# Optimization experiments

Measured on AMD Instinct MI355X. Metric: run time of the kernel, lower is better.

The kernel has to match this reference:

```python
import jax, jax.numpy as jnp
import numpy as np

B, C, H, E, K, QT = 256, 1024, 64, 64, 2, 20000

def _mlp(x, W1, b1, W2, b2):
    # GKT MLP (eval mode: dropout off; batch-norm omitted, see notes)
    return jax.nn.relu(jax.nn.relu(x @ W1 + b1) @ W2 + b2)

def setup_inputs() -> dict:
    key = jax.random.key(0)
    ks = jax.random.split(key, 30)
    s = 0.05  # weight scale to keep pre-clamp activations in a sane range
    xt = jax.random.uniform(ks[0], (B,), dtype=jnp.float32)
    qt = jax.random.randint(ks[1], (B,), 0, QT)
    ht = jax.random.normal(ks[2], (B, C, H), dtype=jnp.float32)
    # binary question->concept incidence, ~4 KCs per question, col 0 forced on
    oh = (jax.random.uniform(ks[3], (QT, C)) < 4.0 / C).astype(jnp.float32)
    oh = oh.at[:, 0].set(1.0)
    qt_kc_one_hot = jnp.concatenate([oh, jnp.zeros((1, C), jnp.float32)], axis=0)  # zero padding row
    kc_embeddings = jax.random.normal(ks[4], (C, E), dtype=jnp.float32) * 0.1
    graphs = jax.random.uniform(ks[5], (K, C, C), dtype=jnp.float32)  # graph_model output
    neigh_weight = jnp.float32(0.8)
    MI = H + E
    Ws1 = jax.random.normal(ks[6], (MI, H), jnp.float32) * s; bs1 = jnp.zeros((H,), jnp.float32)
    Ws2 = jax.random.normal(ks[7], (H, H), jnp.float32) * s;  bs2 = jnp.zeros((H,), jnp.float32)
    Wn1 = jax.random.normal(ks[8], (K, 2 * MI, H), jnp.float32) * s; bn1 = jnp.zeros((K, H), jnp.float32)
    Wn2 = jax.random.normal(ks[9], (K, H, H), jnp.float32) * s;      bn2 = jnp.zeros((K, H), jnp.float32)
    ea_w = jax.random.uniform(ks[10], (C,), dtype=jnp.float32)
    We = jax.random.normal(ks[11], (H, H), jnp.float32) * s; be = jnp.zeros((H,), jnp.float32)
    Wa = jax.random.normal(ks[12], (H, H), jnp.float32) * s; ba = jnp.zeros((H,), jnp.float32)
    W_ih = jax.random.normal(ks[13], (H, 3 * H), jnp.float32) * s; b_ih = jnp.zeros((3 * H,), jnp.float32)
    W_hh = jax.random.normal(ks[14], (H, 3 * H), jnp.float32) * s; b_hh = jnp.zeros((3 * H,), jnp.float32)
    Wp = jax.random.normal(ks[15], (H, 1), jnp.float32) * s; bp = jnp.zeros((1,), jnp.float32)
    return dict(xt=xt, qt=qt, ht=ht, qt_kc_one_hot=qt_kc_one_hot, kc_embeddings=kc_embeddings,
                graphs=graphs, neigh_weight=neigh_weight, Ws1=Ws1, bs1=bs1, Ws2=Ws2, bs2=bs2,
                Wn1=Wn1, bn1=bn1, Wn2=Wn2, bn2=bn2, ea_w=ea_w, We=We, be=be, Wa=Wa, ba=ba,
                W_ih=W_ih, b_ih=b_ih, W_hh=W_hh, b_hh=b_hh, Wp=Wp, bp=bp)

def reference(xt, qt, ht, qt_kc_one_hot, kc_embeddings, graphs, neigh_weight,
              Ws1, bs1, Ws2, bs2, Wn1, bn1, Wn2, bn2, ea_w, We, be, Wa, ba,
              W_ih, b_ih, W_hh, b_hh, Wp, bp):
    # ---- _aggregate: the fusion loops never write back, so tmp_ht = cat(ht, kc_emb)
    mask = qt_kc_one_hot[qt]                                   # [B, C] gather of binary incidence
    kc = jnp.broadcast_to(kc_embeddings[None], (mask.shape[0], C, E))
    tmp_ht = jnp.concatenate([ht, kc], axis=-1)                # [B, C, H+E]
    # ---- _agg_neighbors
    self_ht = tmp_ht * mask[..., None]
    self_feat = jnp.clip(_mlp(self_ht, Ws1, bs1, Ws2, bs2), -10.0, 10.0)
    neigh_ht = jnp.clip(jnp.concatenate([self_ht, tmp_ht], axis=-1), -5.0, 5.0)  # [B,C,2(H+E)]
    # bug-faithful adj: mean of graphs[k] rows over sample 0's active concepts
    a0 = mask[0]                                               # [C]
    denom = jnp.maximum(a0.sum(), 1.0)
    adj = jnp.clip(jnp.einsum('c,kcd->kd', a0, graphs) / denom, -5.0, 5.0)       # [K, C]
    nb = jax.vmap(lambda W1, b1, W2, b2: _mlp(neigh_ht, W1, b1, W2, b2))(Wn1, bn1, Wn2, bn2)
    nb = jnp.clip(nb, -5.0, 5.0)                               # [K, B, C, H]
    w = jnp.clip(neigh_weight, 0.1, 0.9)
    nf = jnp.clip(adj[0][None, :, None] * nb[0], -5.0, 5.0)
    for k in range(1, K):
        nf = jnp.clip(w * nf + (1.0 - w) * adj[k][None, :, None] * nb[k], -5.0, 5.0)
    m_next = jnp.clip(jnp.where(mask[..., None] > 0.5, self_feat, nf), -50.0, 50.0)
    # ---- erase-add gate
    g = ea_w[None, :, None]
    res = m_next - g * jax.nn.sigmoid(m_next @ We + be) * m_next + g * jnp.tanh(m_next @ Wa + ba)
    # ---- GRUCell over flattened (B*C) rows
    gi = res @ W_ih + b_ih
    gh = ht @ W_hh + b_hh
    ir, iz, in_ = jnp.split(gi, 3, axis=-1)
    hr, hz, hn = jnp.split(gh, 3, axis=-1)
    r = jax.nn.sigmoid(ir + hr)
    z = jax.nn.sigmoid(iz + hz)
    n = jnp.tanh(in_ + r * hn)
    h_next = (1.0 - z) * n + z * ht                            # [B, C, H]
    y = jax.nn.sigmoid(h_next @ Wp + bp)[..., 0]               # [B, C]
    return y
```

## Files before the change

kernel.cpp:

```cpp
#include <hip/hip_runtime.h>

#define DEVINL __device__ __forceinline__

typedef __bf16 bf16x8 __attribute__((ext_vector_type(8)));
typedef float  f32x4  __attribute__((ext_vector_type(4)));

static constexpr size_t kAdjOff  = 0;
static constexpr size_t kBiasOff = 8192;
static constexpr size_t kFragOff = 8192 + 786432;

static constexpr int FB_Wn1h0 = 0,  FB_Wn1h1 = 8,  FB_Wn2_0 = 16, FB_Wn2_1 = 24;
static constexpr int FB_Ws1h  = 32, FB_Ws2   = 40, FB_We    = 48, FB_Wa    = 56;
static constexpr int FB_Wih   = 64, FB_Whh   = 88;

DEVINL unsigned short bf16r(float f) {
  unsigned u = __builtin_bit_cast(unsigned, f);
  unsigned r = ((u >> 16) & 1u) + 0x7FFFu;
  return (unsigned short)((u + r) >> 16);
}
DEVINL float sigmoidf_(float x) { return __builtin_amdgcn_rcpf(1.f + __expf(-x)); }
DEVINL float tanhf_(float x)    { return 1.f - 2.f * __builtin_amdgcn_rcpf(1.f + __expf(2.f * x)); }

DEVINL void lds_fence() {
  __builtin_amdgcn_sched_barrier(0x7F);
  __builtin_amdgcn_s_waitcnt(0xC07F);
  __builtin_amdgcn_sched_barrier(0x7F);
}

DEVINL f32x4 mfma16(bf16x8 a, bf16x8 b, f32x4 c) {
  return __builtin_amdgcn_mfma_f32_16x16x32_bf16(a, b, c, 0, 0, 0);
}

DEVINL unsigned clip2_(unsigned x) {
  float lo = __builtin_bit_cast(float, x << 16);
  float hi = __builtin_bit_cast(float, x & 0xFFFF0000u);
  lo = fminf(fmaxf(lo, -5.f), 5.f);
  hi = fminf(fmaxf(hi, -5.f), 5.f);
  return (__builtin_bit_cast(unsigned, lo) >> 16) | (__builtin_bit_cast(unsigned, hi) & 0xFFFF0000u);
}
DEVINL bf16x8 clip5(bf16x8 a) {
  uint4 u = __builtin_bit_cast(uint4, a);
  u.x = clip2_(u.x); u.y = clip2_(u.y); u.z = clip2_(u.z); u.w = clip2_(u.w);
  return __builtin_bit_cast(bf16x8, u);
}

__global__ void prep_adj_kernel(const int* __restrict__ qt, const float* __restrict__ onehot,
                                const float* __restrict__ graphs, float* __restrict__ adjw) {
  __shared__ float a0v[1024];
  __shared__ int   aidx[1024];
  __shared__ int   s_nnz;
  __shared__ float s_den;
  const int tid = threadIdx.x;
  const int k = blockIdx.x >> 2, chunk = blockIdx.x & 3;
  if (tid == 0) { s_nnz = 0; s_den = 0.f; }
  __syncthreads();
  const int q0 = qt[0];
  float lsum = 0.f;
#pragma unroll
  for (int i = 0; i < 4; i++) {
    int c = tid * 4 + i;
    float v = onehot[(size_t)q0 * 1024 + c];
    lsum += v;
    if (v != 0.f) { int p = atomicAdd(&s_nnz, 1); aidx[p] = c; a0v[p] = v; }
  }
#pragma unroll
  for (int off = 32; off >= 1; off >>= 1) lsum += __shfl_xor(lsum, off, 64);
  if ((tid & 63) == 0) atomicAdd(&s_den, lsum);
  __syncthreads();
  const float denom = fmaxf(s_den, 1.f);
  const int nnz = s_nnz;
  const int d = chunk * 256 + tid;
  const float* G = graphs + (size_t)k * 1048576 + d;
  float sum = 0.f;
  for (int j = 0; j < nnz; j++) sum += a0v[j] * G[(size_t)aidx[j] * 1024];
  adjw[k * 1024 + d] = fminf(fmaxf(sum / denom, -5.f), 5.f);
}

__global__ void prep_bias_kernel(const float* __restrict__ kc, const float* __restrict__ Wn1,
                                 const float* __restrict__ bn1, const float* __restrict__ Ws1,
                                 const float* __restrict__ bs1, float* __restrict__ biasTab) {
  int gid = blockIdx.x * 256 + threadIdx.x;
  int j = gid & 63;
  int c = (gid >> 6) & 1023;
  int tab = gid >> 16;
  const float* kcr = kc + (size_t)c * 64;
  float s;
  if (tab < 2) {
    s = bn1[tab * 64 + j];
    const float* W = Wn1 + ((size_t)tab * 256 + 192) * 64 + j;
#pragma unroll 4
    for (int e = 0; e < 64; e++) s += fminf(fmaxf(kcr[e], -5.f), 5.f) * W[(size_t)e * 64];
  } else {
    s = bs1[j];
    const float* W = Ws1 + (size_t)64 * 64 + j;
#pragma unroll 4
    for (int e = 0; e < 64; e++) s += kcr[e] * W[(size_t)e * 64];
  }
  int c16 = c >> 4, rr = c & 3, qq = (c & 15) >> 2, nt = j >> 4;
  int lane = qq * 16 + (j & 15);
  biasTab[(size_t)((((c16 * 3 + tab) * 4 + nt) * 64 + lane)) * 4 + rr] = s;
}

__global__ void prep_wfrag_kernel(const float* __restrict__ Wn1, const float* __restrict__ Wn2,
                                  const float* __restrict__ Ws1, const float* __restrict__ Ws2,
                                  const float* __restrict__ We,  const float* __restrict__ Wa,
                                  const float* __restrict__ Wih, const float* __restrict__ Whh,
                                  uint4* __restrict__ wfrag) {
  const int bid = blockIdx.x, lane = threadIdx.x;
  int mat, ks, nt;
  if (bid < 64) { mat = bid >> 3; ks = (bid >> 2) & 1; nt = bid & 3; }
  else { int f2 = bid - 64; mat = 8 + f2 / 24; int f = f2 % 24; ks = f / 12; nt = f % 12; }
  const float* base = Wn1; int stride = 64;
  switch (mat) {
    case 0: base = Wn1 + (size_t)128 * 64; break;
    case 1: base = Wn1 + (size_t)(256 + 128) * 64; break;
    case 2: base = Wn2; break;
    case 3: base = Wn2 + (size_t)64 * 64; break;
    case 4: base = Ws1; break;
    case 5: base = Ws2; break;
    case 6: base = We; break;
    case 7: base = Wa; break;
    case 8: base = Wih; stride = 192; break;
    case 9: base = Whh; stride = 192; break;
  }
  const int qq = lane >> 4, col = nt * 16 + (lane & 15);
  union { unsigned short u[8]; uint4 v; } tmp;
#pragma unroll
  for (int jj = 0; jj < 8; jj++) {
    int k = ks * 32 + qq * 8 + jj;
    tmp.u[jj] = bf16r(base[(size_t)k * stride + col]);
  }
  wfrag[(size_t)bid * 64 + lane] = tmp.v;
}

__global__ __launch_bounds__(256, 3) void gkt_main_kernel(
    const int* __restrict__ qt, const float* __restrict__ onehot, const float* __restrict__ ht,
    const float* __restrict__ nw, const float* __restrict__ bn2, const float* __restrict__ be,
    const float* __restrict__ ba, const float* __restrict__ bih, const float* __restrict__ bhh,
    const float* __restrict__ Wp, const float* __restrict__ bp, const float* __restrict__ eaw,
    const float* __restrict__ bs2, const float* __restrict__ adjw, const float* __restrict__ biasTab,
    const bf16x8* __restrict__ wfrag, float* __restrict__ out) {
  __shared__ __align__(16) unsigned short hbuf[4][16][72];
  __shared__ __align__(16) float tokp[4][64];
  __shared__ __align__(16) uint4 gfrag[40 * 64];

  const int tid = threadIdx.x;
  const int wv = tid >> 6, lane = tid & 63;
  const int q = lane >> 4, cl = lane & 15;
  const int t0 = (blockIdx.x * 4 + wv) * 16;
  const int b = t0 >> 10, c0 = t0 & 1023, c16 = c0 >> 4;

  unsigned short* hb = &hbuf[wv][0][0];
  float* tp = &tokp[wv][0];

  {
    const uint4* wf4 = (const uint4*)wfrag;
#pragma unroll
    for (int i = 0; i < 10; i++) {
      int f = wv * 10 + i;
      gfrag[f * 64 + lane] = wf4[(64 + f) * 64 + lane];
    }
  }

  if (lane < 16) {
    const int c = c0 + lane;
    tp[lane]      = onehot[(size_t)qt[b] * 1024 + c];
    tp[16 + lane] = adjw[c];
    tp[32 + lane] = adjw[1024 + c];
    tp[48 + lane] = eaw[c];
  }
  {
    const float4* ht4 = (const float4*)ht;
#pragma unroll
    for (int i = 0; i < 4; i++) {
      float4 v = ht4[(size_t)t0 * 16 + i * 64 + lane];
      int e = i * 64 + lane;
      int tok = e >> 4, coll = (e & 15) * 4;
      ushort4 h;
      h.x = bf16r(v.x); h.y = bf16r(v.y); h.z = bf16r(v.z); h.w = bf16r(v.w);
      *(ushort4*)&hbuf[wv][tok][coll] = h;
    }
  }
  __syncthreads();

  const float wmix = fminf(fmaxf(nw[0], 0.1f), 0.9f);

  auto ldA = [&](int ks) -> bf16x8 {
    return *(const bf16x8*)(hb + cl * 72 + ks * 32 + q * 8);
  };
  auto ldB = [&](int frag) -> bf16x8 { return wfrag[frag * 64 + lane]; };
  auto ldG = [&](int fr) -> bf16x8 {
    return (fr < 40) ? *(const bf16x8*)&gfrag[fr * 64 + lane]
                     : wfrag[(64 + fr) * 64 + lane];
  };
  auto ldTP4 = [&](int base) -> f32x4 {
    return *(const f32x4*)(tp + base + q * 4);
  };
  const f32x4* bt4 = (const f32x4*)biasTab;

  bf16x8 xr[2];
#pragma unroll
  for (int ks = 0; ks < 2; ks++) xr[ks] = ldA(ks);
  lds_fence();

  f32x4 nf[4];
  {
    bf16x8 xc[2];
#pragma unroll
    for (int ks = 0; ks < 2; ks++) xc[ks] = clip5(xr[ks]);

#pragma unroll
    for (int k2 = 0; k2 < 2; k2++) {
      f32x4 acc[4];
#pragma unroll
      for (int nt = 0; nt < 4; nt++)
        acc[nt] = bt4[((c16 * 3 + k2) * 4 + nt) * 64 + lane];
#pragma unroll
      for (int ks = 0; ks < 2; ks++)
#pragma unroll
        for (int nt = 0; nt < 4; nt++) {
          bf16x8 bb = ldB((k2 ? FB_Wn1h1 : FB_Wn1h0) + ks * 4 + nt);
          acc[nt] = mfma16(xc[ks], bb, acc[nt]);
        }
#pragma unroll
      for (int nt = 0; nt < 4; nt++)
#pragma unroll
        for (int r = 0; r < 4; r++)
          hb[(q * 4 + r) * 72 + nt * 16 + cl] = bf16r(fmaxf(acc[nt][r], 0.f));
      lds_fence();
      f32x4 acc2[4];
#pragma unroll
      for (int nt = 0; nt < 4; nt++) {
        float bz = bn2[k2 * 64 + nt * 16 + cl];
        acc2[nt] = {bz, bz, bz, bz};
      }
#pragma unroll
      for (int ks = 0; ks < 2; ks++) {
        bf16x8 a0 = ldA(ks);
#pragma unroll
        for (int nt = 0; nt < 4; nt++) {
          bf16x8 bb = ldB((k2 ? FB_Wn2_1 : FB_Wn2_0) + ks * 4 + nt);
          acc2[nt] = mfma16(a0, bb, acc2[nt]);
        }
      }
      lds_fence();
      {
        f32x4 adjv = ldTP4((1 + k2) * 16);
#pragma unroll
        for (int nt = 0; nt < 4; nt++)
#pragma unroll
          for (int r = 0; r < 4; r++) {
            float nb = fminf(fmaxf(acc2[nt][r], 0.f), 5.f);
            float v = adjv[r] * nb;
            if (k2 == 0) nf[nt][r] = wmix * fminf(fmaxf(v, -5.f), 5.f);
            else         nf[nt][r] = fminf(fmaxf(nf[nt][r] + (1.f - wmix) * v, -5.f), 5.f);
          }
      }
    }
  }

  bool anySelf = __any((lane < 16) && (tp[lane] > 0.5f));
  if (anySelf) {
    f32x4 acc[4];
#pragma unroll
    for (int nt = 0; nt < 4; nt++)
      acc[nt] = bt4[((c16 * 3 + 2) * 4 + nt) * 64 + lane];
#pragma unroll
    for (int ks = 0; ks < 2; ks++)
#pragma unroll
      for (int nt = 0; nt < 4; nt++) {
        bf16x8 bb = ldB(FB_Ws1h + ks * 4 + nt);
        acc[nt] = mfma16(xr[ks], bb, acc[nt]);
      }
#pragma unroll
    for (int nt = 0; nt < 4; nt++)
#pragma unroll
      for (int r = 0; r < 4; r++)
        hb[(q * 4 + r) * 72 + nt * 16 + cl] = bf16r(fmaxf(acc[nt][r], 0.f));
    lds_fence();
    f32x4 acc2[4];
#pragma unroll
    for (int nt = 0; nt < 4; nt++) {
      float bz = bs2[nt * 16 + cl];
      acc2[nt] = {bz, bz, bz, bz};
    }
#pragma unroll
    for (int ks = 0; ks < 2; ks++) {
      bf16x8 a0 = ldA(ks);
#pragma unroll
      for (int nt = 0; nt < 4; nt++) {
        bf16x8 bb = ldB(FB_Ws2 + ks * 4 + nt);
        acc2[nt] = mfma16(a0, bb, acc2[nt]);
      }
    }
    lds_fence();
    {
      f32x4 mk = ldTP4(0);
#pragma unroll
      for (int nt = 0; nt < 4; nt++)
#pragma unroll
        for (int r = 0; r < 4; r++) {
          float sf = fminf(fmaxf(acc2[nt][r], 0.f), 10.f);
          nf[nt][r] = (mk[r] > 0.5f) ? sf : nf[nt][r];
        }
    }
  }

#pragma unroll
  for (int nt = 0; nt < 4; nt++)
#pragma unroll
    for (int r = 0; r < 4; r++)
      hb[(q * 4 + r) * 72 + nt * 16 + cl] = bf16r(nf[nt][r]);
  lds_fence();
  bf16x8 mf[2];
#pragma unroll
  for (int ks = 0; ks < 2; ks++) mf[ks] = ldA(ks);
  lds_fence();
  {
    f32x4 accE[4];
#pragma unroll
    for (int nt = 0; nt < 4; nt++) {
      float bz = be[nt * 16 + cl];
      accE[nt] = {bz, bz, bz, bz};
    }
#pragma unroll
    for (int ks = 0; ks < 2; ks++)
#pragma unroll
      for (int nt = 0; nt < 4; nt++) {
        bf16x8 bb = ldB(FB_We + ks * 4 + nt);
        accE[nt] = mfma16(mf[ks], bb, accE[nt]);
      }
    {
      f32x4 gv = ldTP4(48);
#pragma unroll
      for (int nt = 0; nt < 4; nt++)
#pragma unroll
        for (int r = 0; r < 4; r++) {
          float m = nf[nt][r];
          nf[nt][r] = m - gv[r] * sigmoidf_(accE[nt][r]) * m;
        }
    }
    f32x4 accA[4];
#pragma unroll
    for (int nt = 0; nt < 4; nt++) {
      float bz = ba[nt * 16 + cl];
      accA[nt] = {bz, bz, bz, bz};
    }
#pragma unroll
    for (int ks = 0; ks < 2; ks++)
#pragma unroll
      for (int nt = 0; nt < 4; nt++) {
        bf16x8 bb = ldB(FB_Wa + ks * 4 + nt);
        accA[nt] = mfma16(mf[ks], bb, accA[nt]);
      }
    {
      f32x4 gv = ldTP4(48);
#pragma unroll
      for (int nt = 0; nt < 4; nt++)
#pragma unroll
        for (int r = 0; r < 4; r++)
          nf[nt][r] += gv[r] * tanhf_(accA[nt][r]);
    }
  }

#pragma unroll
  for (int nt = 0; nt < 4; nt++)
#pragma unroll
    for (int r = 0; r < 4; r++)
      hb[(q * 4 + r) * 72 + nt * 16 + cl] = bf16r(nf[nt][r]);
  lds_fence();
  bf16x8 rf[2];
#pragma unroll
  for (int ks = 0; ks < 2; ks++) rf[ks] = ldA(ks);

  f32x4 gR[4], gZ[4], gN[4], gH[4];
#pragma unroll
  for (int nt = 0; nt < 4; nt++) {
    int col = nt * 16 + cl;
    float brz = bih[col] + bhh[col];
    float bzz = bih[64 + col] + bhh[64 + col];
    float bnn = bih[128 + col];
    float bhn = bhh[128 + col];
    gR[nt] = {brz, brz, brz, brz};
    gZ[nt] = {bzz, bzz, bzz, bzz};
    gN[nt] = {bnn, bnn, bnn, bnn};
    gH[nt] = {bhn, bhn, bhn, bhn};
  }
#pragma unroll
  for (int ks = 0; ks < 2; ks++)
#pragma unroll
    for (int nt = 0; nt < 4; nt++) {
      bf16x8 bi_r = ldG(ks * 12 + nt);
      bf16x8 bh_r = ldG(24 + ks * 12 + nt);
      bf16x8 bi_z = ldG(ks * 12 + 4 + nt);
      bf16x8 bh_z = ldG(24 + ks * 12 + 4 + nt);
      bf16x8 bi_n = ldG(ks * 12 + 8 + nt);
      bf16x8 bh_n = ldG(24 + ks * 12 + 8 + nt);
      gR[nt] = mfma16(rf[ks], bi_r, gR[nt]);
      gR[nt] = mfma16(xr[ks], bh_r, gR[nt]);
      gZ[nt] = mfma16(rf[ks], bi_z, gZ[nt]);
      gZ[nt] = mfma16(xr[ks], bh_z, gZ[nt]);
      gN[nt] = mfma16(rf[ks], bi_n, gN[nt]);
      gH[nt] = mfma16(xr[ks], bh_n, gH[nt]);
    }

  float wp4[4];
#pragma unroll
  for (int nt = 0; nt < 4; nt++) wp4[nt] = Wp[nt * 16 + cl];
  const float bpv = bp[0];

#pragma unroll
  for (int r = 0; r < 4; r++) {
    int tok = q * 4 + r;
    float part = 0.f;
#pragma unroll
    for (int nt = 0; nt < 4; nt++) {
      float rr = sigmoidf_(gR[nt][r]);
      float zz = sigmoidf_(gZ[nt][r]);
      float nval = tanhf_(gN[nt][r] + rr * gH[nt][r]);
      float htv = ht[(size_t)(t0 + tok) * 64 + nt * 16 + cl];
      float hnx = (1.f - zz) * nval + zz * htv;
      part += hnx * wp4[nt];
    }
    part += __shfl_xor(part, 1, 64);
    part += __shfl_xor(part, 2, 64);
    part += __shfl_xor(part, 4, 64);
    part += __shfl_xor(part, 8, 64);
    if (cl == 0) out[t0 + tok] = sigmoidf_(part + bpv);
  }
}

extern "C" void kernel_launch(void* const* d_in, const int* in_sizes, int n_in,
                              void* d_out, int out_size, void* d_ws, size_t ws_size,
                              hipStream_t stream) {
  const int*   qt     = (const int*)d_in[1];
  const float* ht     = (const float*)d_in[2];
  const float* onehot = (const float*)d_in[3];
  const float* kc     = (const float*)d_in[4];
  const float* graphs = (const float*)d_in[5];
  const float* nw     = (const float*)d_in[6];
  const float* Ws1    = (const float*)d_in[7];
  const float* bs1    = (const float*)d_in[8];
  const float* Ws2    = (const float*)d_in[9];
  const float* bs2    = (const float*)d_in[10];
  const float* Wn1    = (const float*)d_in[11];
  const float* bn1    = (const float*)d_in[12];
  const float* Wn2    = (const float*)d_in[13];
  const float* bn2    = (const float*)d_in[14];
  const float* eaw    = (const float*)d_in[15];
  const float* We     = (const float*)d_in[16];
  const float* be     = (const float*)d_in[17];
  const float* Wa     = (const float*)d_in[18];
  const float* ba     = (const float*)d_in[19];
  const float* Wih    = (const float*)d_in[20];
  const float* bih    = (const float*)d_in[21];
  const float* Whh    = (const float*)d_in[22];
  const float* bhh    = (const float*)d_in[23];
  const float* Wp     = (const float*)d_in[24];
  const float* bp     = (const float*)d_in[25];
  float* out = (float*)d_out;

  float* adjw    = (float*)((char*)d_ws + kAdjOff);
  float* biasTab = (float*)((char*)d_ws + kBiasOff);
  uint4* wfragU  = (uint4*)((char*)d_ws + kFragOff);

  prep_adj_kernel<<<8, 256, 0, stream>>>(qt, onehot, graphs, adjw);
  prep_bias_kernel<<<768, 256, 0, stream>>>(kc, Wn1, bn1, Ws1, bs1, biasTab);
  prep_wfrag_kernel<<<112, 64, 0, stream>>>(Wn1, Wn2, Ws1, Ws2, We, Wa, Wih, Whh, wfragU);
  gkt_main_kernel<<<4096, 256, 0, stream>>>(qt, onehot, ht, nw, bn2, be, ba, bih, bhh,
                                            Wp, bp, eaw, bs2, adjw, biasTab,
                                            (const bf16x8*)wfragU, out);
}
```

Baseline: 270.7 us.

## Transpose activation scratch layout and use ds_read_b64_tr_b16 with packed bf16 stores

```diff
diff --git a/kernel.cpp b/kernel.cpp
--- a/kernel.cpp
+++ b/kernel.cpp
@@ -4,6 +4,7 @@
 
 typedef __bf16 bf16x8 __attribute__((ext_vector_type(8)));
 typedef float  f32x4  __attribute__((ext_vector_type(4)));
+typedef unsigned u32x2 __attribute__((ext_vector_type(2)));
 
 static constexpr size_t kAdjOff  = 0;
 static constexpr size_t kBiasOff = 8192;
@@ -21,10 +22,10 @@
 DEVINL float sigmoidf_(float x) { return __builtin_amdgcn_rcpf(1.f + __expf(-x)); }
 DEVINL float tanhf_(float x)    { return 1.f - 2.f * __builtin_amdgcn_rcpf(1.f + __expf(2.f * x)); }
 
-DEVINL void lds_fence() {
-  __builtin_amdgcn_sched_barrier(0x7F);
-  __builtin_amdgcn_s_waitcnt(0xC07F);
-  __builtin_amdgcn_sched_barrier(0x7F);
+DEVINL unsigned pkbf(float a, float b) {
+  unsigned d;
+  asm("v_cvt_pk_bf16_f32 %0, %1, %2" : "=v"(d) : "v"(a), "v"(b));
+  return d;
 }
 
 DEVINL f32x4 mfma16(bf16x8 a, bf16x8 b, f32x4 c) {
@@ -42,6 +43,23 @@
   uint4 u = __builtin_bit_cast(uint4, a);
   u.x = clip2_(u.x); u.y = clip2_(u.y); u.z = clip2_(u.z); u.w = clip2_(u.w);
   return __builtin_bit_cast(bf16x8, u);
+}
+
+DEVINL void ldA2_tr(unsigned addr, bf16x8& a0, bf16x8& a1) {
+  u32x2 r0, r1, r2, r3;
+  asm volatile(
+      "ds_read_b64_tr_b16 %0, %4\n\t"
+      "ds_read_b64_tr_b16 %1, %4 offset:512\n\t"
+      "ds_read_b64_tr_b16 %2, %4 offset:1024\n\t"
+      "ds_read_b64_tr_b16 %3, %4 offset:1536\n\t"
+      "s_waitcnt lgkmcnt(0)"
+      : "=&v"(r0), "=&v"(r1), "=&v"(r2), "=&v"(r3)
+      : "v"(addr)
+      : "memory");
+  uint4 u0{r0.x, r0.y, r1.x, r1.y};
+  uint4 u1{r2.x, r2.y, r3.x, r3.y};
+  a0 = __builtin_bit_cast(bf16x8, u0);
+  a1 = __builtin_bit_cast(bf16x8, u1);
 }
 
 __global__ void prep_adj_kernel(const int* __restrict__ qt, const float* __restrict__ onehot,
@@ -127,7 +145,7 @@
   union { unsigned short u[8]; uint4 v; } tmp;
 #pragma unroll
   for (int jj = 0; jj < 8; jj++) {
-    int k = ks * 32 + qq * 8 + jj;
+    int k = ks * 32 + ((jj < 4) ? (qq * 4 + jj) : (16 + qq * 4 + (jj - 4)));
     tmp.u[jj] = bf16r(base[(size_t)k * stride + col]);
   }
   wfrag[(size_t)bid * 64 + lane] = tmp.v;
@@ -140,7 +158,7 @@
     const float* __restrict__ Wp, const float* __restrict__ bp, const float* __restrict__ eaw,
     const float* __restrict__ bs2, const float* __restrict__ adjw, const float* __restrict__ biasTab,
     const bf16x8* __restrict__ wfrag, float* __restrict__ out) {
-  __shared__ __align__(16) unsigned short hbuf[4][16][72];
+  __shared__ __align__(128) unsigned short hbuf[4][64][16];
   __shared__ __align__(16) float tokp[4][64];
   __shared__ __align__(16) uint4 gfrag[40 * 64];
 
@@ -152,6 +170,7 @@
 
   unsigned short* hb = &hbuf[wv][0][0];
   float* tp = &tokp[wv][0];
+  const unsigned hbA = (unsigned)(size_t)hb + lane * 8;
 
   {
     const uint4* wf4 = (const uint4*)wfrag;
@@ -175,19 +194,17 @@
     for (int i = 0; i < 4; i++) {
       float4 v = ht4[(size_t)t0 * 16 + i * 64 + lane];
       int e = i * 64 + lane;
-      int tok = e >> 4, coll = (e & 15) * 4;
-      ushort4 h;
-      h.x = bf16r(v.x); h.y = bf16r(v.y); h.z = bf16r(v.z); h.w = bf16r(v.w);
-      *(ushort4*)&hbuf[wv][tok][coll] = h;
+      int tok = e >> 4, fb = (e & 15) * 4;
+      hbuf[wv][fb + 0][tok] = bf16r(v.x);
+      hbuf[wv][fb + 1][tok] = bf16r(v.y);
+      hbuf[wv][fb + 2][tok] = bf16r(v.z);
+      hbuf[wv][fb + 3][tok] = bf16r(v.w);
     }
   }
   __syncthreads();
 
   const float wmix = fminf(fmaxf(nw[0], 0.1f), 0.9f);
 
-  auto ldA = [&](int ks) -> bf16x8 {
-    return *(const bf16x8*)(hb + cl * 72 + ks * 32 + q * 8);
-  };
   auto ldB = [&](int frag) -> bf16x8 { return wfrag[frag * 64 + lane]; };
   auto ldG = [&](int fr) -> bf16x8 {
     return (fr < 40) ? *(const bf16x8*)&gfrag[fr * 64 + lane]
@@ -196,12 +213,15 @@
   auto ldTP4 = [&](int base) -> f32x4 {
     return *(const f32x4*)(tp + base + q * 4);
   };
+  auto packRow = [&](int nt, float v0, float v1, float v2, float v3) {
+    unsigned long long d = (unsigned long long)pkbf(v0, v1) |
+                           ((unsigned long long)pkbf(v2, v3) << 32);
+    *(unsigned long long*)&hbuf[wv][nt * 16 + cl][q * 4] = d;
+  };
   const f32x4* bt4 = (const f32x4*)biasTab;
 
   bf16x8 xr[2];
-#pragma unroll
-  for (int ks = 0; ks < 2; ks++) xr[ks] = ldA(ks);
-  lds_fence();
+  ldA2_tr(hbA, xr[0], xr[1]);
 
   f32x4 nf[4];
   {
@@ -224,10 +244,10 @@
         }
 #pragma unroll
       for (int nt = 0; nt < 4; nt++)
-#pragma unroll
-        for (int r = 0; r < 4; r++)
-          hb[(q * 4 + r) * 72 + nt * 16 + cl] = bf16r(fmaxf(acc[nt][r], 0.f));
-      lds_fence();
+        packRow(nt, fmaxf(acc[nt][0], 0.f), fmaxf(acc[nt][1], 0.f),
+                    fmaxf(acc[nt][2], 0.f), fmaxf(acc[nt][3], 0.f));
+      bf16x8 a0, a1;
+      ldA2_tr(hbA, a0, a1);
       f32x4 acc2[4];
 #pragma unroll
       for (int nt = 0; nt < 4; nt++) {
@@ -235,15 +255,10 @@
         acc2[nt] = {bz, bz, bz, bz};
       }
 #pragma unroll
-      for (int ks = 0; ks < 2; ks++) {
-        bf16x8 a0 = ldA(ks);
-#pragma unroll
-        for (int nt = 0; nt < 4; nt++) {
-          bf16x8 bb = ldB((k2 ? FB_Wn2_1 : FB_Wn2_0) + ks * 4 + nt);
-          acc2[nt] = mfma16(a0, bb, acc2[nt]);
-        }
-      }
-      lds_fence();
+      for (int nt = 0; nt < 4; nt++) {
+        acc2[nt] = mfma16(a0, ldB((k2 ? FB_Wn2_1 : FB_Wn2_0) + nt), acc2[nt]);
+        acc2[nt] = mfma16(a1, ldB((k2 ? FB_Wn2_1 : FB_Wn2_0) + 4 + nt), acc2[nt]);
+      }
       {
         f32x4 adjv = ldTP4((1 + k2) * 16);
 #pragma unroll
@@ -274,10 +289,10 @@
       }
 #pragma unroll
     for (int nt = 0; nt < 4; nt++)
-#pragma unroll
-      for (int r = 0; r < 4; r++)
-        hb[(q * 4 + r) * 72 + nt * 16 + cl] = bf16r(fmaxf(acc[nt][r], 0.f));
-    lds_fence();
+      packRow(nt, fmaxf(acc[nt][0], 0.f), fmaxf(acc[nt][1], 0.f),
+                  fmaxf(acc[nt][2], 0.f), fmaxf(acc[nt][3], 0.f));
+    bf16x8 a0, a1;
+    ldA2_tr(hbA, a0, a1);
     f32x4 acc2[4];
 #pragma unroll
     for (int nt = 0; nt < 4; nt++) {
@@ -285,15 +300,10 @@
       acc2[nt] = {bz, bz, bz, bz};
     }
 #pragma unroll
-    for (int ks = 0; ks < 2; ks++) {
-      bf16x8 a0 = ldA(ks);
-#pragma unroll
-      for (int nt = 0; nt < 4; nt++) {
-        bf16x8 bb = ldB(FB_Ws2 + ks * 4 + nt);
-        acc2[nt] = mfma16(a0, bb, acc2[nt]);
-      }
-    }
-    lds_fence();
+    for (int nt = 0; nt < 4; nt++) {
+      acc2[nt] = mfma16(a0, ldB(FB_Ws2 + nt), acc2[nt]);
+      acc2[nt] = mfma16(a1, ldB(FB_Ws2 + 4 + nt), acc2[nt]);
+    }
     {
       f32x4 mk = ldTP4(0);
 #pragma unroll
@@ -308,14 +318,9 @@
 
 #pragma unroll
   for (int nt = 0; nt < 4; nt++)
-#pragma unroll
-    for (int r = 0; r < 4; r++)
-      hb[(q * 4 + r) * 72 + nt * 16 + cl] = bf16r(nf[nt][r]);
-  lds_fence();
+    packRow(nt, nf[nt][0], nf[nt][1], nf[nt][2], nf[nt][3]);
   bf16x8 mf[2];
-#pragma unroll
-  for (int ks = 0; ks < 2; ks++) mf[ks] = ldA(ks);
-  lds_fence();
+  ldA2_tr(hbA, mf[0], mf[1]);
   {
     f32x4 accE[4];
 #pragma unroll
@@ -365,13 +370,9 @@
 
 #pragma unroll
   for (int nt = 0; nt < 4; nt++)
-#pragma unroll
-    for (int r = 0; r < 4; r++)
-      hb[(q * 4 + r) * 72 + nt * 16 + cl] = bf16r(nf[nt][r]);
-  lds_fence();
+    packRow(nt, nf[nt][0], nf[nt][1], nf[nt][2], nf[nt][3]);
   bf16x8 rf[2];
-#pragma unroll
-  for (int ks = 0; ks < 2; ks++) rf[ks] = ldA(ks);
+  ldA2_tr(hbA, rf[0], rf[1]);
 
   f32x4 gR[4], gZ[4], gN[4], gH[4];
 #pragma unroll
```

After: 270.0 us. About the same (-0.2%).
